# Kernel optimization log

Hardware: AMD Instinct MI355X
Metric: run time of the kernel (lower is better)

## Reference

```python
import jax, jax.numpy as jnp
import numpy as np

BINWIDTHS = (5000, 1000, 500, 200, 100, 50, 25)
WINDOW = (0, 200000)
TOTAL = WINDOW[1] - WINDOW[0]

def _level_shapes():
    shapes = []
    cw = TOTAL
    for bw in BINWIDTHS:
        nb = cw // bw
        ns = TOTAL // (bw * nb)
        shapes.append((ns, nb))
        cw = bw
    return shapes

LEVEL_SHAPES = _level_shapes()          # [(1,40),(40,5),(200,2),(500,2),(1000,2),(2000,2),(4000,2)]
NBINS = [ns * nb for ns, nb in LEVEL_SHAPES]
N_FINAL = TOTAL // BINWIDTHS[-1]        # 8000

N_REGIONS = 500
N_CLUSTERS = 20
N_REGIONS_OI = 256
N_CELLS = 10000
N_CUTS = 500000
DELTA_P_SCALE = 1.5


def setup_inputs() -> dict:
    key = jax.random.key(0)
    ks = jax.random.split(key, 32)
    inp = {}
    inp["components"] = jax.random.normal(ks[0], (N_CLUSTERS, N_CLUSTERS), jnp.float32)
    for lvl, (ns, nb) in enumerate(LEVEL_SHAPES):
        inp[f"w_bias_{lvl}"] = jax.random.normal(ks[1 + lvl], (N_REGIONS, ns, nb), jnp.float32) * 0.05
        inp[f"w_delta_{lvl}"] = jax.random.normal(ks[10 + lvl], (N_REGIONS, N_CLUSTERS, ns * nb), jnp.float32) * 0.02
    inp["regions_oi"] = jax.random.randint(ks[20], (N_REGIONS_OI,), 0, N_REGIONS)
    inp["local_region_ix"] = jax.random.randint(ks[21], (N_CUTS,), 0, N_REGIONS_OI)
    inp["local_cell_ix"] = jax.random.randint(ks[22], (N_CUTS,), 0, N_CELLS)
    inp["clustering_indices"] = jax.random.randint(ks[23], (N_CELLS,), 0, N_CLUSTERS)
    inp["coordinates"] = jax.random.randint(ks[24], (N_CUTS,), WINDOW[0], WINDOW[1])
    return inp


def _calculate_w(components, w_biases, w_deltas, regions_oi):
    R = regions_oi.shape[0]
    C = components.shape[1]
    scale = jnp.float32(DELTA_P_SCALE)
    log_scale = jnp.log(scale)
    half_log_2pi = jnp.float32(0.5 * np.log(2.0 * np.pi))
    w = jnp.zeros((R, C, N_FINAL), jnp.float32)
    kl = jnp.float32(0.0)
    for lvl, (ns, nb) in enumerate(LEVEL_SHAPES):
        wb = w_biases[lvl][regions_oi]                    # (R, ns, nb) irregular gather
        Wd = w_deltas[lvl][regions_oi]                    # (R, C, ns*nb) irregular gather
        # MultiLinear: einsum('ab,cad->cbd', components, W)
        wd = jnp.einsum('ab,cad->cbd', components, Wd)    # (R, C, ns*nb)
        wd = wd.reshape(R, C, ns, nb)
        w_level = (wb[:, None, :, :] + wd).reshape(R, C, NBINS[lvl])
        rep = N_FINAL // NBINS[lvl]
        w = (w.reshape(R, C, NBINS[lvl], rep) + w_level[..., None]).reshape(R, C, N_FINAL)
        # Normal(0, scale).log_prob(wd), summed
        kl = kl + jnp.sum(-0.5 * (wd / scale) ** 2 - log_scale - half_log_2pi)
    w = jax.nn.log_softmax(w, axis=-1) - jnp.log(jnp.float32(BINWIDTHS[-1]))
    return w, kl


def reference(components, w_bias_0, w_bias_1, w_bias_2, w_bias_3, w_bias_4, w_bias_5, w_bias_6,
              w_delta_0, w_delta_1, w_delta_2, w_delta_3, w_delta_4, w_delta_5, w_delta_6,
              regions_oi, local_region_ix, local_cell_ix, clustering_indices, coordinates):
    w_biases = [w_bias_0, w_bias_1, w_bias_2, w_bias_3, w_bias_4, w_bias_5, w_bias_6]
    w_deltas = [w_delta_0, w_delta_1, w_delta_2, w_delta_3, w_delta_4, w_delta_5, w_delta_6]
    w, kl = _calculate_w(components, w_biases, w_deltas, regions_oi)
    coords = jnp.clip(coordinates, WINDOW[0], WINDOW[1] - 1) - WINDOW[0]
    bin_ix = coords // BINWIDTHS[-1]
    cluster_ix = clustering_indices[local_cell_ix]
    likelihood = w[local_region_ix, cluster_ix, bin_ix]   # (N_CUTS,)
    return likelihood, kl
```

## Files before the change

kernel.cpp:

```cpp
#include <hip/hip_runtime.h>
#include <hip/hip_bf16.h>
#include <math.h>


#define NROI 256
#define NC 20
#define NFINAL 8000
#define NCUTS 500000
#define TB 256
#define NTILE 32

__global__ void k_init(const float* __restrict__ comp,
                       float* __restrict__ g2, float* __restrict__ compT,
                       float* __restrict__ kl)
{
    const int tid = threadIdx.x;
    if (tid == 0) kl[0] = (float)(-80076800.0 * 1.3244036413128371);
    for (int i = tid; i < 400; i += 256) {
        const int a = i / 20, b = i % 20;
        float s = 0.f;
#pragma unroll
        for (int c = 0; c < 20; c++) s += comp[a * 20 + c] * comp[b * 20 + c];
        g2[i] = (b < a) ? 0.f : (b == a ? s : 2.f * s);
        compT[i] = comp[b * 20 + a];
    }
}

__global__ __launch_bounds__(256, 2) void k_main(
    const float* __restrict__ compT, const float* __restrict__ g2,
    const float* __restrict__ wb0, const float* __restrict__ wd0,
    const float* __restrict__ wb1, const float* __restrict__ wd1,
    const float* __restrict__ wb2, const float* __restrict__ wd2,
    const float* __restrict__ wb3, const float* __restrict__ wd3,
    const float* __restrict__ wb4, const float* __restrict__ wd4,
    const float* __restrict__ wb5, const float* __restrict__ wd5,
    const float* __restrict__ wb6, const float* __restrict__ wd6,
    const int* __restrict__ regions_oi,
    __hip_bfloat16* __restrict__ w2,
    float* __restrict__ s_part, float* __restrict__ kl_out)
{
    __shared__ float U_sh[20 * TB];
    __shared__ float bias_sh[TB];
    __shared__ float klp[4];

    const int tid = threadIdx.x;
    const int wv = tid >> 6, lane = tid & 63;
    const int r = blockIdx.x >> 5;
    const int tile = blockIdx.x & 31;
    const int base = tile << 8;
    const int r0 = regions_oi[r];

    const float* __restrict__ p6 = wd6 + (size_t)r0 * (20 * 8000);
    const float* __restrict__ p5 = wd5 + (size_t)r0 * (20 * 4000);
    const float* __restrict__ p4 = wd4 + (size_t)r0 * (20 * 2000);
    const float* __restrict__ p3 = wd3 + (size_t)r0 * (20 * 1000);
    const float* __restrict__ p2 = wd2 + (size_t)r0 * (20 * 400);
    const float* __restrict__ p1 = wd1 + (size_t)r0 * (20 * 200);
    const float* __restrict__ p0 = wd0 + (size_t)r0 * (20 * 40);
    const float* __restrict__ b6 = wb6 + (size_t)r0 * 8000;
    const float* __restrict__ b5 = wb5 + (size_t)r0 * 4000;
    const float* __restrict__ b4 = wb4 + (size_t)r0 * 2000;
    const float* __restrict__ b3 = wb3 + (size_t)r0 * 1000;
    const float* __restrict__ b2 = wb2 + (size_t)r0 * 400;
    const float* __restrict__ b1 = wb1 + (size_t)r0 * 200;
    const float* __restrict__ b0 = wb0 + (size_t)r0 * 40;

#pragma unroll 1
    for (int it = 0; it < 6; it++) {
        const int u = it * 256 + tid;
        if (u >= 1344) break;
        if (u < 1280) {
            const int a = u >> 6, jq = u & 63;
            const int j = base + 4 * jq;
            float4 uu = make_float4(0.f, 0.f, 0.f, 0.f);
            if (j < NFINAL) {
                const float4 v6 = *(const float4*)(p6 + (size_t)a * 8000 + j);
                const float2 v5 = *(const float2*)(p5 + a * 4000 + (j >> 1));
                const float sc = p4[a * 2000 + (j >> 2)] + p3[a * 1000 + (j >> 3)]
                               + p2[a * 400 + j / 20] + p1[a * 200 + j / 40]
                               + p0[a * 40 + j / 200];
                const float c01 = sc + v5.x, c23 = sc + v5.y;
                uu.x = v6.x + c01; uu.y = v6.y + c01;
                uu.z = v6.z + c23; uu.w = v6.w + c23;
            }
            *(float4*)(&U_sh[a * TB + 4 * jq]) = uu;
        } else {
            const int jq = u - 1280;
            const int j = base + 4 * jq;
            float4 uu = make_float4(0.f, 0.f, 0.f, 0.f);
            if (j < NFINAL) {
                const float4 v6 = *(const float4*)(b6 + j);
                const float2 v5 = *(const float2*)(b5 + (j >> 1));
                const float sc = b4[j >> 2] + b3[j >> 3] + b2[j / 20]
                               + b1[j / 40] + b0[j / 200];
                const float c01 = sc + v5.x, c23 = sc + v5.y;
                uu.x = v6.x + c01; uu.y = v6.y + c01;
                uu.z = v6.z + c23; uu.w = v6.w + c23;
            }
            *(float4*)(&bias_sh[4 * jq]) = uu;
        }
    }
    __syncthreads();

    const int cb = __builtin_amdgcn_readfirstlane(wv * 5);
    const float* __restrict__ cc = compT + cb * 20;
    const int j = base + 4 * lane;
    const bool ok = j < NFINAL;
    const float4 bi = *(const float4*)(&bias_sh[4 * lane]);

    {
        float4 a0 = bi, a1 = bi, a2 = bi;
#pragma unroll
        for (int a = 0; a < 20; a++) {
            const float4 u = *(const float4*)(&U_sh[a * TB + 4 * lane]);
            const float f0 = cc[a], f1 = cc[20 + a], f2 = cc[40 + a];
            a0.x += f0 * u.x; a0.y += f0 * u.y; a0.z += f0 * u.z; a0.w += f0 * u.w;
            a1.x += f1 * u.x; a1.y += f1 * u.y; a1.z += f1 * u.z; a1.w += f1 * u.w;
            a2.x += f2 * u.x; a2.y += f2 * u.y; a2.z += f2 * u.z; a2.w += f2 * u.w;
        }
        float4 accs[3] = {a0, a1, a2};
#pragma unroll
        for (int k = 0; k < 3; k++) {
            float se = 0.f;
            if (ok) {
                const float4 acc = accs[k];
                union { __hip_bfloat162 h2[2]; uint2 u2; } pk;
                pk.h2[0] = __float22bfloat162_rn(make_float2(acc.x, acc.y));
                pk.h2[1] = __float22bfloat162_rn(make_float2(acc.z, acc.w));
                *(uint2*)(w2 + (size_t)(r * 20 + cb + k) * 8000 + j) = pk.u2;
                se = __expf(acc.x) + __expf(acc.y) + __expf(acc.z) + __expf(acc.w);
            }
#pragma unroll
            for (int off = 32; off > 0; off >>= 1) se += __shfl_down(se, off, 64);
            if (lane == 0) s_part[((size_t)r * NTILE + tile) * 20 + cb + k] = se;
        }
    }
    {
        float4 a0 = bi, a1 = bi;
#pragma unroll
        for (int a = 0; a < 20; a++) {
            const float4 u = *(const float4*)(&U_sh[a * TB + 4 * lane]);
            const float f0 = cc[60 + a], f1 = cc[80 + a];
            a0.x += f0 * u.x; a0.y += f0 * u.y; a0.z += f0 * u.z; a0.w += f0 * u.w;
            a1.x += f1 * u.x; a1.y += f1 * u.y; a1.z += f1 * u.z; a1.w += f1 * u.w;
        }
        float4 accs[2] = {a0, a1};
#pragma unroll
        for (int k = 0; k < 2; k++) {
            float se = 0.f;
            if (ok) {
                const float4 acc = accs[k];
                union { __hip_bfloat162 h2[2]; uint2 u2; } pk;
                pk.h2[0] = __float22bfloat162_rn(make_float2(acc.x, acc.y));
                pk.h2[1] = __float22bfloat162_rn(make_float2(acc.z, acc.w));
                *(uint2*)(w2 + (size_t)(r * 20 + cb + 3 + k) * 8000 + j) = pk.u2;
                se = __expf(acc.x) + __expf(acc.y) + __expf(acc.z) + __expf(acc.w);
            }
#pragma unroll
            for (int off = 32; off > 0; off >>= 1) se += __shfl_down(se, off, 64);
            if (lane == 0) s_part[((size_t)r * NTILE + tile) * 20 + cb + 3 + k] = se;
        }
    }

    float q = 0.f;
#pragma unroll 1
    for (int it = 0; it < 2; it++) {
        const int u = it * 256 + tid;
        if (u >= 480) break;
        const float* P; int K, col;
        if (u < 256)      { P = p6; K = 8000; col = base + u; }
        else if (u < 384) { P = p5; K = 4000; col = (base >> 1) + (u - 256); }
        else if (u < 448) { P = p4; K = 2000; col = (base >> 2) + (u - 384); }
        else              { P = p3; K = 1000; col = (base >> 3) + (u - 448); }
        if (col < K) {
            float x[20];
#pragma unroll
            for (int a = 0; a < 20; a++) x[a] = P[(size_t)a * K + col];
#pragma unroll
            for (int a = 0; a < 20; a++) {
                float t = g2[a * 21] * x[a];
#pragma unroll
                for (int b = a + 1; b < 20; b++) t += g2[a * 20 + b] * x[b];
                q += x[a] * t;
            }
        }
    }
#pragma unroll
    for (int off = 32; off > 0; off >>= 1) q += __shfl_down(q, off, 64);
    if (lane == 0) klp[wv] = q;
    __syncthreads();
    if (tid == 0)
        atomicAdd(kl_out, (klp[0] + klp[1] + klp[2] + klp[3]) * (-0.5f / 2.25f));
}

__global__ __launch_bounds__(256, 2) void k_klc(
    const float* __restrict__ g2,
    const float* __restrict__ wd0, const float* __restrict__ wd1,
    const float* __restrict__ wd2,
    const int* __restrict__ regions_oi, float* __restrict__ kl_out)
{
    __shared__ float klp[4];
    const int tid = threadIdx.x;
    const int r0 = regions_oi[blockIdx.x];
    const float* __restrict__ p2 = wd2 + (size_t)r0 * (20 * 400);
    const float* __restrict__ p1 = wd1 + (size_t)r0 * (20 * 200);
    const float* __restrict__ p0 = wd0 + (size_t)r0 * (20 * 40);

    float q = 0.f;
#pragma unroll 1
    for (int it = 0; it < 3; it++) {
        const int u = it * 256 + tid;
        if (u >= 640) break;
        const float* P; int K, col;
        if (u < 400)      { P = p2; K = 400; col = u; }
        else if (u < 600) { P = p1; K = 200; col = u - 400; }
        else              { P = p0; K = 40;  col = u - 600; }
        float x[20];
#pragma unroll
        for (int a = 0; a < 20; a++) x[a] = P[a * K + col];
#pragma unroll
        for (int a = 0; a < 20; a++) {
            float t = g2[a * 21] * x[a];
#pragma unroll
            for (int b = a + 1; b < 20; b++) t += g2[a * 20 + b] * x[b];
            q += x[a] * t;
        }
    }
#pragma unroll
    for (int off = 32; off > 0; off >>= 1) q += __shfl_down(q, off, 64);
    if ((tid & 63) == 0) klp[tid >> 6] = q;
    __syncthreads();
    if (tid == 0)
        atomicAdd(kl_out, (klp[0] + klp[1] + klp[2] + klp[3]) * (-0.5f / 2.25f));
}

__global__ void k_sub(const float* __restrict__ s_part, float* __restrict__ sub)
{
    const int i = blockIdx.x * 256 + threadIdx.x;
    if (i >= NROI * NC) return;
    const int r = i / 20, c = i % 20;
    float s = 0.f;
#pragma unroll 1
    for (int t = 0; t < NTILE; t++) s += s_part[(size_t)(r * NTILE + t) * 20 + c];
    sub[i] = logf(s) + 3.2188758248682006f;
}

__global__ void k_gather(const int* __restrict__ lri, const int* __restrict__ lci,
                         const int* __restrict__ cli, const int* __restrict__ coords,
                         const __hip_bfloat16* __restrict__ w2,
                         const float* __restrict__ sub,
                         float* __restrict__ out)
{
    const int i = blockIdx.x * 256 + threadIdx.x;
    if (i >= NCUTS) return;
    const int r = lri[i];
    const int c = cli[lci[i]];
    int co = coords[i];
    co = co < 0 ? 0 : (co > 199999 ? 199999 : co);
    const int bin = co / 25;
    const int rc = r * 20 + c;
    out[i] = __bfloat162float(w2[(size_t)rc * 8000 + bin]) - sub[rc];
}

extern "C" void kernel_launch(void* const* d_in, const int* in_sizes, int n_in,
                              void* d_out, int out_size, void* d_ws, size_t ws_size,
                              hipStream_t stream)
{
    const float* comp = (const float*)d_in[0];
    const float* wb[7];
    const float* wd[7];
    if (in_sizes[2] == 400000) {
        for (int l = 0; l < 7; l++) { wb[l] = (const float*)d_in[1 + 2 * l]; wd[l] = (const float*)d_in[2 + 2 * l]; }
    } else {
        for (int l = 0; l < 7; l++) { wb[l] = (const float*)d_in[1 + l]; wd[l] = (const float*)d_in[8 + l]; }
    }
    const int* regions_oi = (const int*)d_in[15];
    const int* lri   = (const int*)d_in[16];
    const int* lci   = (const int*)d_in[17];
    const int* cli   = (const int*)d_in[18];
    const int* coords= (const int*)d_in[19];
    float* out = (float*)d_out;

    __hip_bfloat16* w2 = (__hip_bfloat16*)d_ws;
    float* s_part = (float*)(w2 + (size_t)NROI * NC * NFINAL);
    float* sub    = s_part + (size_t)NROI * NTILE * 20;
    float* g2buf  = sub + NROI * NC;
    float* compT  = g2buf + 400;
    const size_t need = (size_t)NROI * NC * NFINAL * 2
                      + ((size_t)NROI * NTILE * 20 + NROI * NC + 800) * sizeof(float);
    if (ws_size < need) return;

    k_init<<<1, 256, 0, stream>>>(comp, g2buf, compT, out + NCUTS);
    k_main<<<NROI * NTILE, 256, 0, stream>>>(compT, g2buf,
        wb[0], wd[0], wb[1], wd[1], wb[2], wd[2], wb[3], wd[3],
        wb[4], wd[4], wb[5], wd[5], wb[6], wd[6],
        regions_oi, w2, s_part, out + NCUTS);
    k_klc<<<NROI, 256, 0, stream>>>(g2buf, wd[0], wd[1], wd[2],
        regions_oi, out + NCUTS);
    k_sub<<<(NROI * NC + 255) / 256, 256, 0, stream>>>(s_part, sub);
    k_gather<<<(NCUTS + 255) / 256, 256, 0, stream>>>(lri, lci, cli, coords,
        w2, sub, out);
}
```

Baseline: 196.5 us.

## Process four tiles per block with double-buffered register prefetch of inputs

Each block of the main kernel now handles four consecutive 256-column tiles of a region instead of one, which cuts the grid size by four. The next tile's level-6/5 delta and bias data is loaded into registers while the current tile's matmul, softmax partials and KL work run, then written into a second shared-memory buffer. Bias rows are folded into the shared tile as a 21st row. The intent is to hide global load latency and amortize per-block setup, at the cost of more registers and shared memory and fewer blocks to spread across CUs.

```diff
diff --git a/kernel.cpp b/kernel.cpp
--- a/kernel.cpp
+++ b/kernel.cpp
@@ -9,6 +9,10 @@
 #define NCUTS 500000
 #define TB 256
 #define NTILE 32
+#define TPB 4
+#define NOCT (NTILE / TPB)
+#define NROWS 21
+#define NUNITS (NROWS * 64)
 
 __global__ void k_init(const float* __restrict__ comp,
                        float* __restrict__ g2, float* __restrict__ compT,
@@ -39,15 +43,14 @@
     __hip_bfloat16* __restrict__ w2,
     float* __restrict__ s_part, float* __restrict__ kl_out)
 {
-    __shared__ float U_sh[20 * TB];
-    __shared__ float bias_sh[TB];
+    __shared__ float U_sh[2][NROWS * TB];
     __shared__ float klp[4];
 
     const int tid = threadIdx.x;
     const int wv = tid >> 6, lane = tid & 63;
-    const int r = blockIdx.x >> 5;
-    const int tile = blockIdx.x & 31;
-    const int base = tile << 8;
+    const int r = blockIdx.x >> 3;
+    const int oct = blockIdx.x & 7;
+    const int t0 = oct * TPB;
     const int r0 = regions_oi[r];
 
     const float* __restrict__ p6 = wd6 + (size_t)r0 * (20 * 8000);
@@ -65,126 +68,161 @@
     const float* __restrict__ b1 = wb1 + (size_t)r0 * 200;
     const float* __restrict__ b0 = wb0 + (size_t)r0 * 40;
 
-#pragma unroll 1
-    for (int it = 0; it < 6; it++) {
-        const int u = it * 256 + tid;
-        if (u >= 1344) break;
-        if (u < 1280) {
-            const int a = u >> 6, jq = u & 63;
-            const int j = base + 4 * jq;
-            float4 uu = make_float4(0.f, 0.f, 0.f, 0.f);
-            if (j < NFINAL) {
-                const float4 v6 = *(const float4*)(p6 + (size_t)a * 8000 + j);
-                const float2 v5 = *(const float2*)(p5 + a * 4000 + (j >> 1));
-                const float sc = p4[a * 2000 + (j >> 2)] + p3[a * 1000 + (j >> 3)]
-                               + p2[a * 400 + j / 20] + p1[a * 200 + j / 40]
-                               + p0[a * 40 + j / 200];
-                const float c01 = sc + v5.x, c23 = sc + v5.y;
-                uu.x = v6.x + c01; uu.y = v6.y + c01;
-                uu.z = v6.z + c23; uu.w = v6.w + c23;
-            }
-            *(float4*)(&U_sh[a * TB + 4 * jq]) = uu;
-        } else {
-            const int jq = u - 1280;
-            const int j = base + 4 * jq;
-            float4 uu = make_float4(0.f, 0.f, 0.f, 0.f);
-            if (j < NFINAL) {
-                const float4 v6 = *(const float4*)(b6 + j);
-                const float2 v5 = *(const float2*)(b5 + (j >> 1));
-                const float sc = b4[j >> 2] + b3[j >> 3] + b2[j / 20]
-                               + b1[j / 40] + b0[j / 200];
-                const float c01 = sc + v5.x, c23 = sc + v5.y;
-                uu.x = v6.x + c01; uu.y = v6.y + c01;
-                uu.z = v6.z + c23; uu.w = v6.w + c23;
-            }
-            *(float4*)(&bias_sh[4 * jq]) = uu;
-        }
-    }
-    __syncthreads();
+    float4 r6[6];
+    float2 r5[6];
+
+    auto LOADR = [&](int tl) {
+#pragma unroll
+        for (int k = 0; k < 6; k++) {
+            const int u = tid + (k << 8);
+            if (u < NUNITS) {
+                const int a = u >> 6, jq = u & 63;
+                const int j = (tl << 8) + 4 * jq;
+                const float* q6 = (a < 20) ? p6 + (size_t)a * 8000 : b6;
+                const float* q5 = (a < 20) ? p5 + (size_t)a * 4000 : b5;
+                if (j < NFINAL) {
+                    r6[k] = *(const float4*)(q6 + j);
+                    r5[k] = *(const float2*)(q5 + (j >> 1));
+                } else {
+                    r6[k] = make_float4(0.f, 0.f, 0.f, 0.f);
+                    r5[k] = make_float2(0.f, 0.f);
+                }
+            }
+        }
+    };
+
+    auto WRITEF = [&](int buf, int tl) {
+#pragma unroll
+        for (int k = 0; k < 6; k++) {
+            const int u = tid + (k << 8);
+            if (u < NUNITS) {
+                const int a = u >> 6, jq = u & 63;
+                const int j = (tl << 8) + 4 * jq;
+                const float *q4, *q3, *q2, *q1, *q0;
+                if (a < 20) {
+                    q4 = p4 + (size_t)a * 2000; q3 = p3 + (size_t)a * 1000;
+                    q2 = p2 + (size_t)a * 400;  q1 = p1 + (size_t)a * 200;
+                    q0 = p0 + (size_t)a * 40;
+                } else {
+                    q4 = b4; q3 = b3; q2 = b2; q1 = b1; q0 = b0;
+                }
+                float sc = 0.f;
+                if (j < NFINAL)
+                    sc = q4[j >> 2] + q3[j >> 3] + q2[j / 20] + q1[j / 40]
+                       + q0[j / 200];
+                const float c01 = sc + r5[k].x, c23 = sc + r5[k].y;
+                float4 uu;
+                uu.x = r6[k].x + c01; uu.y = r6[k].y + c01;
+                uu.z = r6[k].z + c23; uu.w = r6[k].w + c23;
+                *(float4*)(&U_sh[buf][a * TB + 4 * jq]) = uu;
+            }
+        }
+    };
 
     const int cb = __builtin_amdgcn_readfirstlane(wv * 5);
     const float* __restrict__ cc = compT + cb * 20;
-    const int j = base + 4 * lane;
-    const bool ok = j < NFINAL;
-    const float4 bi = *(const float4*)(&bias_sh[4 * lane]);
-
-    {
-        float4 a0 = bi, a1 = bi, a2 = bi;
-#pragma unroll
-        for (int a = 0; a < 20; a++) {
-            const float4 u = *(const float4*)(&U_sh[a * TB + 4 * lane]);
-            const float f0 = cc[a], f1 = cc[20 + a], f2 = cc[40 + a];
-            a0.x += f0 * u.x; a0.y += f0 * u.y; a0.z += f0 * u.z; a0.w += f0 * u.w;
-            a1.x += f1 * u.x; a1.y += f1 * u.y; a1.z += f1 * u.z; a1.w += f1 * u.w;
-            a2.x += f2 * u.x; a2.y += f2 * u.y; a2.z += f2 * u.z; a2.w += f2 * u.w;
-        }
-        float4 accs[3] = {a0, a1, a2};
-#pragma unroll
-        for (int k = 0; k < 3; k++) {
-            float se = 0.f;
-            if (ok) {
-                const float4 acc = accs[k];
-                union { __hip_bfloat162 h2[2]; uint2 u2; } pk;
-                pk.h2[0] = __float22bfloat162_rn(make_float2(acc.x, acc.y));
-                pk.h2[1] = __float22bfloat162_rn(make_float2(acc.z, acc.w));
-                *(uint2*)(w2 + (size_t)(r * 20 + cb + k) * 8000 + j) = pk.u2;
-                se = __expf(acc.x) + __expf(acc.y) + __expf(acc.z) + __expf(acc.w);
-            }
-#pragma unroll
-            for (int off = 32; off > 0; off >>= 1) se += __shfl_down(se, off, 64);
-            if (lane == 0) s_part[((size_t)r * NTILE + tile) * 20 + cb + k] = se;
+
+    auto PAF = [&](int buf, int tl) {
+        const int j = (tl << 8) + 4 * lane;
+        const bool ok = j < NFINAL;
+        const float4 bi = *(const float4*)(&U_sh[buf][20 * TB + 4 * lane]);
+        {
+            float4 a0 = bi, a1 = bi, a2 = bi;
+#pragma unroll
+            for (int a = 0; a < 20; a++) {
+                const float4 u = *(const float4*)(&U_sh[buf][a * TB + 4 * lane]);
+                const float f0 = cc[a], f1 = cc[20 + a], f2 = cc[40 + a];
+                a0.x += f0 * u.x; a0.y += f0 * u.y; a0.z += f0 * u.z; a0.w += f0 * u.w;
+                a1.x += f1 * u.x; a1.y += f1 * u.y; a1.z += f1 * u.z; a1.w += f1 * u.w;
+                a2.x += f2 * u.x; a2.y += f2 * u.y; a2.z += f2 * u.z; a2.w += f2 * u.w;
+            }
+            float4 accs[3] = {a0, a1, a2};
+#pragma unroll
+            for (int k = 0; k < 3; k++) {
+                float se = 0.f;
+                if (ok) {
+                    const float4 acc = accs[k];
+                    union { __hip_bfloat162 h2[2]; uint2 u2; } pk;
+                    pk.h2[0] = __float22bfloat162_rn(make_float2(acc.x, acc.y));
+                    pk.h2[1] = __float22bfloat162_rn(make_float2(acc.z, acc.w));
+                    *(uint2*)(w2 + (size_t)(r * 20 + cb + k) * 8000 + j) = pk.u2;
+                    se = __expf(acc.x) + __expf(acc.y) + __expf(acc.z) + __expf(acc.w);
+                }
+#pragma unroll
+                for (int off = 32; off > 0; off >>= 1) se += __shfl_down(se, off, 64);
+                if (lane == 0) s_part[((size_t)r * NTILE + tl) * 20 + cb + k] = se;
+            }
+        }
+        {
+            float4 a0 = bi, a1 = bi;
+#pragma unroll
+            for (int a = 0; a < 20; a++) {
+                const float4 u = *(const float4*)(&U_sh[buf][a * TB + 4 * lane]);
+                const float f0 = cc[60 + a], f1 = cc[80 + a];
+                a0.x += f0 * u.x; a0.y += f0 * u.y; a0.z += f0 * u.z; a0.w += f0 * u.w;
+                a1.x += f1 * u.x; a1.y += f1 * u.y; a1.z += f1 * u.z; a1.w += f1 * u.w;
+            }
+            float4 accs[2] = {a0, a1};
+#pragma unroll
+            for (int k = 0; k < 2; k++) {
+                float se = 0.f;
+                if (ok) {
+                    const float4 acc = accs[k];
+                    union { __hip_bfloat162 h2[2]; uint2 u2; } pk;
+                    pk.h2[0] = __float22bfloat162_rn(make_float2(acc.x, acc.y));
+                    pk.h2[1] = __float22bfloat162_rn(make_float2(acc.z, acc.w));
+                    *(uint2*)(w2 + (size_t)(r * 20 + cb + 3 + k) * 8000 + j) = pk.u2;
+                    se = __expf(acc.x) + __expf(acc.y) + __expf(acc.z) + __expf(acc.w);
+                }
+#pragma unroll
+                for (int off = 32; off > 0; off >>= 1) se += __shfl_down(se, off, 64);
+                if (lane == 0) s_part[((size_t)r * NTILE + tl) * 20 + cb + 3 + k] = se;
+            }
+        }
+    };
+
+    float q = 0.f;
+    auto PQF = [&](int tl) {
+        const int base = tl << 8;
+#pragma unroll 1
+        for (int it = 0; it < 2; it++) {
+            const int u = it * 256 + tid;
+            if (u >= 480) break;
+            const float* P; int K, col;
+            if (u < 256)      { P = p6; K = 8000; col = base + u; }
+            else if (u < 384) { P = p5; K = 4000; col = (base >> 1) + (u - 256); }
+            else if (u < 448) { P = p4; K = 2000; col = (base >> 2) + (u - 384); }
+            else              { P = p3; K = 1000; col = (base >> 3) + (u - 448); }
+            if (col < K) {
+                float x[20];
+#pragma unroll
+                for (int a = 0; a < 20; a++) x[a] = P[(size_t)a * K + col];
+#pragma unroll
+                for (int a = 0; a < 20; a++) {
+                    float t = g2[a * 21] * x[a];
+#pragma unroll
+                    for (int b = a + 1; b < 20; b++) t += g2[a * 20 + b] * x[b];
+                    q += x[a] * t;
+                }
+            }
+        }
+    };
+
+    LOADR(t0);
+    WRITEF(0, t0);
+    __syncthreads();
+#pragma unroll 1
+    for (int t = 0; t < TPB; t++) {
+        const int tl = t0 + t;
+        if (t < TPB - 1) LOADR(tl + 1);
+        PAF(t & 1, tl);
+        PQF(tl);
+        if (t < TPB - 1) {
+            WRITEF((t + 1) & 1, tl + 1);
+            __syncthreads();
         }
     }
-    {
-        float4 a0 = bi, a1 = bi;
-#pragma unroll
-        for (int a = 0; a < 20; a++) {
-            const float4 u = *(const float4*)(&U_sh[a * TB + 4 * lane]);
-            const float f0 = cc[60 + a], f1 = cc[80 + a];
-            a0.x += f0 * u.x; a0.y += f0 * u.y; a0.z += f0 * u.z; a0.w += f0 * u.w;
-            a1.x += f1 * u.x; a1.y += f1 * u.y; a1.z += f1 * u.z; a1.w += f1 * u.w;
-        }
-        float4 accs[2] = {a0, a1};
-#pragma unroll
-        for (int k = 0; k < 2; k++) {
-            float se = 0.f;
-            if (ok) {
-                const float4 acc = accs[k];
-                union { __hip_bfloat162 h2[2]; uint2 u2; } pk;
-                pk.h2[0] = __float22bfloat162_rn(make_float2(acc.x, acc.y));
-                pk.h2[1] = __float22bfloat162_rn(make_float2(acc.z, acc.w));
-                *(uint2*)(w2 + (size_t)(r * 20 + cb + 3 + k) * 8000 + j) = pk.u2;
-                se = __expf(acc.x) + __expf(acc.y) + __expf(acc.z) + __expf(acc.w);
-            }
-#pragma unroll
-            for (int off = 32; off > 0; off >>= 1) se += __shfl_down(se, off, 64);
-            if (lane == 0) s_part[((size_t)r * NTILE + tile) * 20 + cb + 3 + k] = se;
-        }
-    }
-
-    float q = 0.f;
-#pragma unroll 1
-    for (int it = 0; it < 2; it++) {
-        const int u = it * 256 + tid;
-        if (u >= 480) break;
-        const float* P; int K, col;
-        if (u < 256)      { P = p6; K = 8000; col = base + u; }
-        else if (u < 384) { P = p5; K = 4000; col = (base >> 1) + (u - 256); }
-        else if (u < 448) { P = p4; K = 2000; col = (base >> 2) + (u - 384); }
-        else              { P = p3; K = 1000; col = (base >> 3) + (u - 448); }
-        if (col < K) {
-            float x[20];
-#pragma unroll
-            for (int a = 0; a < 20; a++) x[a] = P[(size_t)a * K + col];
-#pragma unroll
-            for (int a = 0; a < 20; a++) {
-                float t = g2[a * 21] * x[a];
-#pragma unroll
-                for (int b = a + 1; b < 20; b++) t += g2[a * 20 + b] * x[b];
-                q += x[a] * t;
-            }
-        }
-    }
+
 #pragma unroll
     for (int off = 32; off > 0; off >>= 1) q += __shfl_down(q, off, 64);
     if (lane == 0) klp[wv] = q;
@@ -291,7 +329,7 @@
     if (ws_size < need) return;
 
     k_init<<<1, 256, 0, stream>>>(comp, g2buf, compT, out + NCUTS);
-    k_main<<<NROI * NTILE, 256, 0, stream>>>(compT, g2buf,
+    k_main<<<NROI * NOCT, 256, 0, stream>>>(compT, g2buf,
         wb[0], wd[0], wb[1], wd[1], wb[2], wd[2], wb[3], wd[3],
         wb[4], wd[4], wb[5], wd[5], wb[6], wd[6],
         regions_oi, w2, s_part, out + NCUTS);
```

Result: slower. 323.0 us (+64.3%).

## Use bf16 MFMA for component mixing and KL quadratic form in main kernel

Applied to the files above, without the earlier changes.

Replaces the scalar FMA loops that mix the 20 components into per-cluster weights with bf16 16x16x32 MFMA instructions, staging the summed per-bin values transposed in LDS as bf16. The KL quadratic form is also computed with MFMA, as a Gram matrix of the level 3-6 deltas contracted against the full components Gram matrix, instead of per-thread triangular loops. Per-cluster exp sums are reduced through shared atomics. The inputs are rounded to bf16 before the matmuls, which costs precision in both the likelihood and the KL sum, and the B operand for the mixing MFMA is read as row-strided 16-byte LDS fragments.

```diff
diff --git a/kernel.cpp b/kernel.cpp
--- a/kernel.cpp
+++ b/kernel.cpp
@@ -9,10 +9,21 @@
 #define NCUTS 500000
 #define TB 256
 #define NTILE 32
+#define XSTR 488
+#define UTSTR 40
+
+typedef __attribute__((ext_vector_type(8))) short bf16x8;
+typedef __attribute__((ext_vector_type(4))) float f32x4;
+
+static __device__ __forceinline__ ushort bfr(float x) {
+    union { __hip_bfloat16 h; ushort u; } v;
+    v.h = __float2bfloat16(x);
+    return v.u;
+}
 
 __global__ void k_init(const float* __restrict__ comp,
-                       float* __restrict__ g2, float* __restrict__ compT,
-                       float* __restrict__ kl)
+                       float* __restrict__ g2, float* __restrict__ gfull,
+                       ushort* __restrict__ compPad, float* __restrict__ kl)
 {
     const int tid = threadIdx.x;
     if (tid == 0) kl[0] = (float)(-80076800.0 * 1.3244036413128371);
@@ -22,12 +33,22 @@
 #pragma unroll
         for (int c = 0; c < 20; c++) s += comp[a * 20 + c] * comp[b * 20 + c];
         g2[i] = (b < a) ? 0.f : (b == a ? s : 2.f * s);
-        compT[i] = comp[b * 20 + a];
+    }
+    for (int i = tid; i < 1024; i += 256) {
+        const int rr = i >> 5, cc = i & 31;
+        float s = 0.f;
+        if (rr < 20 && cc < 20) {
+#pragma unroll
+            for (int c = 0; c < 20; c++) s += comp[rr * 20 + c] * comp[cc * 20 + c];
+        }
+        gfull[i] = s;
+        const float v = (rr < 20 && cc < 20) ? comp[cc * 20 + rr] : 0.f;
+        compPad[i] = bfr(v);
     }
 }
 
 __global__ __launch_bounds__(256, 2) void k_main(
-    const float* __restrict__ compT, const float* __restrict__ g2,
+    const float* __restrict__ gfull, const ushort* __restrict__ compPad,
     const float* __restrict__ wb0, const float* __restrict__ wd0,
     const float* __restrict__ wb1, const float* __restrict__ wd1,
     const float* __restrict__ wb2, const float* __restrict__ wd2,
@@ -39,12 +60,15 @@
     __hip_bfloat16* __restrict__ w2,
     float* __restrict__ s_part, float* __restrict__ kl_out)
 {
-    __shared__ float U_sh[20 * TB];
-    __shared__ float bias_sh[TB];
-    __shared__ float klp[4];
+    __shared__ ushort Xsh[32 * XSTR];
+    __shared__ ushort Utsh[TB * UTSTR];
+    __shared__ float biasf[TB];
+    __shared__ float sexp_sh[20];
+    __shared__ float klp[3];
 
     const int tid = threadIdx.x;
-    const int wv = tid >> 6, lane = tid & 63;
+    const int wv = tid >> 6, ln = tid & 63;
+    const int l15 = ln & 15, lg = ln >> 4;
     const int r = blockIdx.x >> 5;
     const int tile = blockIdx.x & 31;
     const int base = tile << 8;
@@ -65,132 +89,132 @@
     const float* __restrict__ b1 = wb1 + (size_t)r0 * 200;
     const float* __restrict__ b0 = wb0 + (size_t)r0 * 40;
 
+    if (tid < 20) sexp_sh[tid] = 0.f;
+    if (tid < 3) klp[tid] = 0.f;
+
+#pragma unroll 1
+    for (int it = 0; it < 8; it++) {
+        const int u = it * 256 + tid;
+        if (u >= 2012) break;
+        if (u < 1280) *(uint4*)&Utsh[u * 8] = make_uint4(0, 0, 0, 0);
+        else          *(uint4*)&Xsh[20 * XSTR + (u - 1280) * 8] = make_uint4(0, 0, 0, 0);
+    }
+    __syncthreads();
+
 #pragma unroll 1
     for (int it = 0; it < 6; it++) {
         const int u = it * 256 + tid;
         if (u >= 1344) break;
-        if (u < 1280) {
-            const int a = u >> 6, jq = u & 63;
-            const int j = base + 4 * jq;
-            float4 uu = make_float4(0.f, 0.f, 0.f, 0.f);
-            if (j < NFINAL) {
-                const float4 v6 = *(const float4*)(p6 + (size_t)a * 8000 + j);
-                const float2 v5 = *(const float2*)(p5 + a * 4000 + (j >> 1));
-                const float sc = p4[a * 2000 + (j >> 2)] + p3[a * 1000 + (j >> 3)]
-                               + p2[a * 400 + j / 20] + p1[a * 200 + j / 40]
-                               + p0[a * 40 + j / 200];
-                const float c01 = sc + v5.x, c23 = sc + v5.y;
-                uu.x = v6.x + c01; uu.y = v6.y + c01;
-                uu.z = v6.z + c23; uu.w = v6.w + c23;
+        const int a = u >> 6, jq = u & 63;
+        const int j = base + 4 * jq;
+        const float *q6, *q5, *q4, *q3, *q2, *q1, *q0;
+        if (a < 20) {
+            q6 = p6 + (size_t)a * 8000; q5 = p5 + a * 4000; q4 = p4 + a * 2000;
+            q3 = p3 + a * 1000; q2 = p2 + a * 400; q1 = p1 + a * 200; q0 = p0 + a * 40;
+        } else { q6 = b6; q5 = b5; q4 = b4; q3 = b3; q2 = b2; q1 = b1; q0 = b0; }
+        float4 r6 = make_float4(0.f, 0.f, 0.f, 0.f);
+        float2 r5 = make_float2(0.f, 0.f);
+        float s4 = 0.f, s3 = 0.f, s2 = 0.f, s1 = 0.f, s0 = 0.f;
+        if (j < NFINAL) {
+            r6 = *(const float4*)(q6 + j);
+            r5 = *(const float2*)(q5 + (j >> 1));
+            s4 = q4[j >> 2]; s3 = q3[j >> 3]; s2 = q2[j / 20];
+            s1 = q1[j / 40]; s0 = q0[j / 200];
+        }
+        const float sc = s4 + s3 + s2 + s1 + s0;
+        const float c01 = sc + r5.x, c23 = sc + r5.y;
+        const float u0 = r6.x + c01, u1 = r6.y + c01;
+        const float u2 = r6.z + c23, u3 = r6.w + c23;
+        if (a < 20) {
+            *(ushort4*)&Xsh[a * XSTR + 4 * jq] =
+                make_ushort4(bfr(r6.x), bfr(r6.y), bfr(r6.z), bfr(r6.w));
+            *(ushort2*)&Xsh[a * XSTR + 256 + 2 * jq] =
+                make_ushort2(bfr(r5.x), bfr(r5.y));
+            Xsh[a * XSTR + 384 + jq] = bfr(s4);
+            if (!(jq & 1)) Xsh[a * XSTR + 448 + (jq >> 1)] = bfr(s3);
+            Utsh[(4 * jq + 0) * UTSTR + a] = bfr(u0);
+            Utsh[(4 * jq + 1) * UTSTR + a] = bfr(u1);
+            Utsh[(4 * jq + 2) * UTSTR + a] = bfr(u2);
+            Utsh[(4 * jq + 3) * UTSTR + a] = bfr(u3);
+        } else {
+            *(float4*)&biasf[4 * jq] = make_float4(u0, u1, u2, u3);
+        }
+    }
+    __syncthreads();
+
+    if (wv < 3) {
+        const int mt = (wv == 0) ? 0 : 1;
+        const int nt = (wv == 2) ? 1 : 0;
+        const int rowA = mt * 16 + l15;
+        const int rowB = nt * 16 + l15;
+        const int kb = lg * 8;
+        f32x4 acc = {0.f, 0.f, 0.f, 0.f};
+#pragma unroll 1
+        for (int ch = 0; ch < 15; ch++) {
+            bf16x8 fa = *(const bf16x8*)&Xsh[rowA * XSTR + ch * 32 + kb];
+            bf16x8 fb = *(const bf16x8*)&Xsh[rowB * XSTR + ch * 32 + kb];
+            acc = __builtin_amdgcn_mfma_f32_16x16x32_bf16(fa, fb, acc, 0, 0, 0);
+        }
+        float qp = 0.f;
+#pragma unroll
+        for (int reg = 0; reg < 4; reg++) {
+            const int row = mt * 16 + lg * 4 + reg;
+            const int col = nt * 16 + l15;
+            qp += gfull[row * 32 + col] * acc[reg];
+        }
+        if (wv == 1) qp *= 2.f;
+#pragma unroll
+        for (int off = 32; off > 0; off >>= 1) qp += __shfl_down(qp, off, 64);
+        if (ln == 0) klp[wv] = qp;
+    }
+
+    bf16x8 fA0 = *(const bf16x8*)&compPad[l15 * 32 + lg * 8];
+    bf16x8 fA1 = *(const bf16x8*)&compPad[(16 + l15) * 32 + lg * 8];
+    float sA[4] = {0.f, 0.f, 0.f, 0.f};
+    float sB[4] = {0.f, 0.f, 0.f, 0.f};
+#pragma unroll 1
+    for (int t = 0; t < 4; t++) {
+        const int nt = 4 * t + wv;
+        bf16x8 fB = *(const bf16x8*)&Utsh[(nt * 16 + l15) * UTSTR + lg * 8];
+        const f32x4 z = {0.f, 0.f, 0.f, 0.f};
+        f32x4 c0 = __builtin_amdgcn_mfma_f32_16x16x32_bf16(fA0, fB, z, 0, 0, 0);
+        f32x4 c1 = __builtin_amdgcn_mfma_f32_16x16x32_bf16(fA1, fB, z, 0, 0, 0);
+        const int binl = nt * 16 + l15;
+        const int bin = base + binl;
+        const float bi = biasf[binl];
+        if (bin < NFINAL) {
+#pragma unroll
+            for (int reg = 0; reg < 4; reg++) {
+                const int c = lg * 4 + reg;
+                const float w = bi + c0[reg];
+                w2[(size_t)(r * 20 + c) * 8000 + bin] = __float2bfloat16(w);
+                sA[reg] += __expf(w);
             }
-            *(float4*)(&U_sh[a * TB + 4 * jq]) = uu;
-        } else {
-            const int jq = u - 1280;
-            const int j = base + 4 * jq;
-            float4 uu = make_float4(0.f, 0.f, 0.f, 0.f);
-            if (j < NFINAL) {
-                const float4 v6 = *(const float4*)(b6 + j);
-                const float2 v5 = *(const float2*)(b5 + (j >> 1));
-                const float sc = b4[j >> 2] + b3[j >> 3] + b2[j / 20]
-                               + b1[j / 40] + b0[j / 200];
-                const float c01 = sc + v5.x, c23 = sc + v5.y;
-                uu.x = v6.x + c01; uu.y = v6.y + c01;
-                uu.z = v6.z + c23; uu.w = v6.w + c23;
+            if (lg == 0) {
+#pragma unroll
+                for (int reg = 0; reg < 4; reg++) {
+                    const float w = bi + c1[reg];
+                    w2[(size_t)(r * 20 + 16 + reg) * 8000 + bin] = __float2bfloat16(w);
+                    sB[reg] += __expf(w);
+                }
             }
-            *(float4*)(&bias_sh[4 * jq]) = uu;
-        }
+        }
+    }
+#pragma unroll
+    for (int reg = 0; reg < 4; reg++) {
+        float s = sA[reg];
+        s += __shfl_xor(s, 1, 64); s += __shfl_xor(s, 2, 64);
+        s += __shfl_xor(s, 4, 64); s += __shfl_xor(s, 8, 64);
+        if (l15 == 0) atomicAdd(&sexp_sh[lg * 4 + reg], s);
+        float sb = sB[reg];
+        sb += __shfl_xor(sb, 1, 64); sb += __shfl_xor(sb, 2, 64);
+        sb += __shfl_xor(sb, 4, 64); sb += __shfl_xor(sb, 8, 64);
+        if (ln == 0) atomicAdd(&sexp_sh[16 + reg], sb);
     }
     __syncthreads();
-
-    const int cb = __builtin_amdgcn_readfirstlane(wv * 5);
-    const float* __restrict__ cc = compT + cb * 20;
-    const int j = base + 4 * lane;
-    const bool ok = j < NFINAL;
-    const float4 bi = *(const float4*)(&bias_sh[4 * lane]);
-
-    {
-        float4 a0 = bi, a1 = bi, a2 = bi;
-#pragma unroll
-        for (int a = 0; a < 20; a++) {
-            const float4 u = *(const float4*)(&U_sh[a * TB + 4 * lane]);
-            const float f0 = cc[a], f1 = cc[20 + a], f2 = cc[40 + a];
-            a0.x += f0 * u.x; a0.y += f0 * u.y; a0.z += f0 * u.z; a0.w += f0 * u.w;
-            a1.x += f1 * u.x; a1.y += f1 * u.y; a1.z += f1 * u.z; a1.w += f1 * u.w;
-            a2.x += f2 * u.x; a2.y += f2 * u.y; a2.z += f2 * u.z; a2.w += f2 * u.w;
-        }
-        float4 accs[3] = {a0, a1, a2};
-#pragma unroll
-        for (int k = 0; k < 3; k++) {
-            float se = 0.f;
-            if (ok) {
-                const float4 acc = accs[k];
-                union { __hip_bfloat162 h2[2]; uint2 u2; } pk;
-                pk.h2[0] = __float22bfloat162_rn(make_float2(acc.x, acc.y));
-                pk.h2[1] = __float22bfloat162_rn(make_float2(acc.z, acc.w));
-                *(uint2*)(w2 + (size_t)(r * 20 + cb + k) * 8000 + j) = pk.u2;
-                se = __expf(acc.x) + __expf(acc.y) + __expf(acc.z) + __expf(acc.w);
-            }
-#pragma unroll
-            for (int off = 32; off > 0; off >>= 1) se += __shfl_down(se, off, 64);
-            if (lane == 0) s_part[((size_t)r * NTILE + tile) * 20 + cb + k] = se;
-        }
-    }
-    {
-        float4 a0 = bi, a1 = bi;
-#pragma unroll
-        for (int a = 0; a < 20; a++) {
-            const float4 u = *(const float4*)(&U_sh[a * TB + 4 * lane]);
-            const float f0 = cc[60 + a], f1 = cc[80 + a];
-            a0.x += f0 * u.x; a0.y += f0 * u.y; a0.z += f0 * u.z; a0.w += f0 * u.w;
-            a1.x += f1 * u.x; a1.y += f1 * u.y; a1.z += f1 * u.z; a1.w += f1 * u.w;
-        }
-        float4 accs[2] = {a0, a1};
-#pragma unroll
-        for (int k = 0; k < 2; k++) {
-            float se = 0.f;
-            if (ok) {
-                const float4 acc = accs[k];
-                union { __hip_bfloat162 h2[2]; uint2 u2; } pk;
-                pk.h2[0] = __float22bfloat162_rn(make_float2(acc.x, acc.y));
-                pk.h2[1] = __float22bfloat162_rn(make_float2(acc.z, acc.w));
-                *(uint2*)(w2 + (size_t)(r * 20 + cb + 3 + k) * 8000 + j) = pk.u2;
-                se = __expf(acc.x) + __expf(acc.y) + __expf(acc.z) + __expf(acc.w);
-            }
-#pragma unroll
-            for (int off = 32; off > 0; off >>= 1) se += __shfl_down(se, off, 64);
-            if (lane == 0) s_part[((size_t)r * NTILE + tile) * 20 + cb + 3 + k] = se;
-        }
-    }
-
-    float q = 0.f;
-#pragma unroll 1
-    for (int it = 0; it < 2; it++) {
-        const int u = it * 256 + tid;
-        if (u >= 480) break;
-        const float* P; int K, col;
-        if (u < 256)      { P = p6; K = 8000; col = base + u; }
-        else if (u < 384) { P = p5; K = 4000; col = (base >> 1) + (u - 256); }
-        else if (u < 448) { P = p4; K = 2000; col = (base >> 2) + (u - 384); }
-        else              { P = p3; K = 1000; col = (base >> 3) + (u - 448); }
-        if (col < K) {
-            float x[20];
-#pragma unroll
-            for (int a = 0; a < 20; a++) x[a] = P[(size_t)a * K + col];
-#pragma unroll
-            for (int a = 0; a < 20; a++) {
-                float t = g2[a * 21] * x[a];
-#pragma unroll
-                for (int b = a + 1; b < 20; b++) t += g2[a * 20 + b] * x[b];
-                q += x[a] * t;
-            }
-        }
-    }
-#pragma unroll
-    for (int off = 32; off > 0; off >>= 1) q += __shfl_down(q, off, 64);
-    if (lane == 0) klp[wv] = q;
-    __syncthreads();
+    if (tid < 20) s_part[((size_t)r * NTILE + tile) * 20 + tid] = sexp_sh[tid];
     if (tid == 0)
-        atomicAdd(kl_out, (klp[0] + klp[1] + klp[2] + klp[3]) * (-0.5f / 2.25f));
+        atomicAdd(kl_out, (klp[0] + klp[1] + klp[2]) * (-0.5f / 2.25f));
 }
 
 __global__ __launch_bounds__(256, 2) void k_klc(
@@ -285,13 +309,15 @@
     float* s_part = (float*)(w2 + (size_t)NROI * NC * NFINAL);
     float* sub    = s_part + (size_t)NROI * NTILE * 20;
     float* g2buf  = sub + NROI * NC;
-    float* compT  = g2buf + 400;
+    float* gfull  = g2buf + 400;
+    ushort* compPad = (ushort*)(gfull + 1024);
     const size_t need = (size_t)NROI * NC * NFINAL * 2
-                      + ((size_t)NROI * NTILE * 20 + NROI * NC + 800) * sizeof(float);
+                      + ((size_t)NROI * NTILE * 20 + NROI * NC + 400 + 1024 + 512)
+                        * sizeof(float);
     if (ws_size < need) return;
 
-    k_init<<<1, 256, 0, stream>>>(comp, g2buf, compT, out + NCUTS);
-    k_main<<<NROI * NTILE, 256, 0, stream>>>(compT, g2buf,
+    k_init<<<1, 256, 0, stream>>>(comp, g2buf, gfull, compPad, out + NCUTS);
+    k_main<<<NROI * NTILE, 256, 0, stream>>>(gfull, compPad,
         wb[0], wd[0], wb[1], wd[1], wb[2], wd[2], wb[3], wd[3],
         wb[4], wd[4], wb[5], wd[5], wb[6], wd[6],
         regions_oi, w2, s_part, out + NCUTS);
```

After: 192.6 us. 2.0% less time.
